# Performance work log

Measured on AMD Instinct MI355X. Metric: run time of the kernel, lower is better.

The kernel has to match this reference:

```python
import jax, jax.numpy as jnp
import numpy as np

K = 4
REG_MAX = 32


def setup_inputs() -> dict:
    key = jax.random.key(0)
    ks = jax.random.split(key, 6)
    B, L, C = 8, 100000, 80
    scores = jax.random.normal(ks[0], (B, L, C), dtype=jnp.float32)
    pred_corners = jax.random.normal(ks[1], (B, L, 4 * (REG_MAX + 1)), dtype=jnp.float32)
    in_dim = 4 * (K + 1)  # 20
    hidden = 64
    w1 = jax.random.normal(ks[2], (in_dim, hidden), dtype=jnp.float32) * (1.0 / np.sqrt(in_dim))
    b1 = jax.random.normal(ks[3], (hidden,), dtype=jnp.float32) * 0.01
    w2 = jax.random.normal(ks[4], (hidden, 1), dtype=jnp.float32) * (1.0 / np.sqrt(hidden))
    b2 = jax.random.normal(ks[5], (1,), dtype=jnp.float32) * 0.01
    return {"scores": scores, "pred_corners": pred_corners,
            "w1": w1, "b1": b1, "w2": w2, "b2": b2}


def reference(scores, pred_corners, w1, b1, w2, b2):
    B, L, _ = pred_corners.shape
    # [B, L, 4, reg_max+1]
    prob = jax.nn.softmax(pred_corners.reshape(B, L, 4, REG_MAX + 1), axis=-1)
    topk, _ = jax.lax.top_k(prob, K)                       # [B, L, 4, k]
    stat = jnp.concatenate([topk, topk.mean(-1, keepdims=True)], axis=-1)  # [B, L, 4, k+1]
    stat = stat.reshape(B, L, 4 * (K + 1))                 # [B, L, 20]
    h = jax.nn.silu(stat @ w1 + b1)                        # [B, L, 64]
    quality = h @ w2 + b2                                  # [B, L, 1]
    return scores + quality
```

## Files before the change

### kernel.cpp

```cpp
#include <hip/hip_runtime.h>

#define LOG2E 1.4426950408889634f

typedef __attribute__((address_space(3))) unsigned int lds_u32_t;
typedef const __attribute__((address_space(1))) unsigned int glb_u32_t;

__global__ __launch_bounds__(256, 4) void lqe_fused2(
    const float* __restrict__ scores,
    const float* __restrict__ pred,
    const float* __restrict__ w1,
    const float* __restrict__ b1,
    const float* __restrict__ w2,
    const float* __restrict__ b2,
    float* __restrict__ out)
{
    __shared__ float predS[64 * 132];
    __shared__ float wS[1412];
    __shared__ float qS[64];

    const int t   = threadIdx.x;
    const int bid = blockIdx.x;

    const size_t f4base = (size_t)bid * 1280;
    const float4* sv4 = reinterpret_cast<const float4*>(scores) + f4base;
    float4 sv[5];
#pragma unroll
    for (int k = 0; k < 5; ++k) sv[k] = sv4[t + 256 * k];

    {
        const float* gp  = pred + (size_t)bid * 8448;
        const int wbase  = t & ~63;
        const int lane   = t & 63;
#pragma unroll
        for (int k = 0; k < 8; ++k) {
            const int f4 = 256 * k + wbase;
            __builtin_amdgcn_global_load_lds(
                (glb_u32_t*)(gp + 4 * (f4 + lane)),
                (lds_u32_t*)(predS + 4 * f4),
                16, 0, 0);
        }
        if (t < 64) {
            __builtin_amdgcn_global_load_lds(
                (glb_u32_t*)(gp + 4 * (2048 + lane)),
                (lds_u32_t*)(predS + 4 * 2048),
                16, 0, 0);
        }
    }

#pragma unroll
    for (int k = 0; k < 5; ++k) wS[t + 256 * k] = w1[t + 256 * k];
    if (t < 64)  { wS[1280 + t] = b1[t]; wS[1344 + t] = w2[t]; }
    if (t == 0)  { wS[1408] = b2[0]; }

    __syncthreads();

    const int r = t >> 2;
    const int c = t & 3;
    const float* xp = predS + r * 132 + c * 33;
    float xs[33];
#pragma unroll
    for (int j = 0; j < 33; ++j) xs[j] = xp[j];

    float t0 = -1e30f, t1 = -1e30f, t2 = -1e30f, t3 = -1e30f;
#pragma unroll
    for (int j = 0; j < 33; ++j) {
        float v  = xs[j];
        float r0 = fminf(t0, v);  t0 = fmaxf(t0, v);
        float r1 = fminf(t1, r0); t1 = fmaxf(t1, r0);
        float r2 = fminf(t2, r1); t2 = fmaxf(t2, r1);
        t3 = fmaxf(t3, r2);
    }

    float denom = 0.f;
#pragma unroll
    for (int j = 0; j < 33; ++j)
        denom += __builtin_amdgcn_exp2f((xs[j] - t0) * LOG2E);
    float rd = __builtin_amdgcn_rcpf(denom);

    float s5[5];
    s5[0] = rd;
    s5[1] = __builtin_amdgcn_exp2f((t1 - t0) * LOG2E) * rd;
    s5[2] = __builtin_amdgcn_exp2f((t2 - t0) * LOG2E) * rd;
    s5[3] = __builtin_amdgcn_exp2f((t3 - t0) * LOG2E) * rd;
    s5[4] = (s5[0] + s5[1] + s5[2] + s5[3]) * 0.25f;

    const int qbase = (t & 63) & ~3;
    float stat[20];
#pragma unroll
    for (int i = 0; i < 20; ++i)
        stat[i] = __shfl(s5[i % 5], qbase + i / 5, 64);

    float hacc[16];
    {
        const float4* b1v = reinterpret_cast<const float4*>(wS + 1280 + 16 * c);
#pragma unroll
        for (int k = 0; k < 4; ++k) {
            float4 b = b1v[k];
            hacc[4*k+0] = b.x; hacc[4*k+1] = b.y; hacc[4*k+2] = b.z; hacc[4*k+3] = b.w;
        }
    }
#pragma unroll
    for (int i = 0; i < 20; ++i) {
        const float si = stat[i];
        const float4* wv = reinterpret_cast<const float4*>(wS + i * 64 + 16 * c);
#pragma unroll
        for (int k = 0; k < 4; ++k) {
            float4 w = wv[k];
            hacc[4*k+0] = fmaf(si, w.x, hacc[4*k+0]);
            hacc[4*k+1] = fmaf(si, w.y, hacc[4*k+1]);
            hacc[4*k+2] = fmaf(si, w.z, hacc[4*k+2]);
            hacc[4*k+3] = fmaf(si, w.w, hacc[4*k+3]);
        }
    }

    float q = 0.f;
    {
        const float4* w2v = reinterpret_cast<const float4*>(wS + 1344 + 16 * c);
#pragma unroll
        for (int k = 0; k < 4; ++k) {
            float4 w = w2v[k];
#pragma unroll
            for (int e = 0; e < 4; ++e) {
                float v  = hacc[4*k+e];
                float sg = __builtin_amdgcn_rcpf(1.f + __builtin_amdgcn_exp2f(-v * LOG2E));
                float we = (e == 0) ? w.x : (e == 1) ? w.y : (e == 2) ? w.z : w.w;
                q = fmaf(v * sg, we, q);
            }
        }
    }
    q += __shfl_xor(q, 1, 64);
    q += __shfl_xor(q, 2, 64);
    q += wS[1408];
    if (c == 0) qS[r] = q;
    __syncthreads();

    float4* ov4 = reinterpret_cast<float4*>(out) + f4base;
#pragma unroll
    for (int k = 0; k < 5; ++k) {
        const int idx = t + 256 * k;
        const float qq = qS[idx / 20];
        float4 s = sv[k];
        s.x += qq; s.y += qq; s.z += qq; s.w += qq;
        ov4[idx] = s;
    }
}

extern "C" void kernel_launch(void* const* d_in, const int* in_sizes, int n_in,
                              void* d_out, int out_size, void* d_ws, size_t ws_size,
                              hipStream_t stream) {
    const float* scores = (const float*)d_in[0];
    const float* pred   = (const float*)d_in[1];
    const float* w1     = (const float*)d_in[2];
    const float* b1     = (const float*)d_in[3];
    const float* w2     = (const float*)d_in[4];
    const float* b2     = (const float*)d_in[5];
    float* out = (float*)d_out;

    const int nrows = in_sizes[1] / 132;
    const int grid  = nrows / 64;

    hipLaunchKernelGGL(lqe_fused2, dim3(grid), dim3(256), 0, stream,
                       scores, pred, w1, b1, w2, b2, out);
}
```

Baseline: 176.0 us.

## Convert to persistent grid with double-buffered LDS prefetch of pred tiles

Replaces the one-tile-per-block launch with a persistent grid of 1024 blocks of 128 threads that each loop over 32-row tiles. The next tile's pred data is staged into a second LDS buffer with global_load_lds while the current tile is computed, and manual vmcnt/lgkmcnt waits plus barriers coordinate the buffers. The goal is to overlap memory fetch with the softmax/top-k/MLP work on this bandwidth-bound kernel. The manual waitcnt counting is fragile, and the last tile issues a redundant reload.

New measurement: 202.7 us. +15.2%, slower.

```diff
diff --git a/kernel.cpp b/kernel.cpp
--- a/kernel.cpp
+++ b/kernel.cpp
@@ -1,147 +1,156 @@
 #include <hip/hip_runtime.h>
 
 #define LOG2E 1.4426950408889634f
+#define ROWS  32
+#define BLK   128
+#define PREDF (ROWS * 132)
+#define SCOR4 (ROWS * 20)
 
 typedef __attribute__((address_space(3))) unsigned int lds_u32_t;
 typedef const __attribute__((address_space(1))) unsigned int glb_u32_t;
 
-__global__ __launch_bounds__(256, 4) void lqe_fused2(
+__device__ __forceinline__ void stage_pred(const float* gp, float* buf, int wv, int lane) {
+#pragma unroll
+    for (int k = 0; k < 8; ++k) {
+        const int f4 = wv * 528 + 64 * k;
+        __builtin_amdgcn_global_load_lds((glb_u32_t*)(gp + 4 * f4 + 4 * lane),
+                                         (lds_u32_t*)(buf + 4 * f4), 16, 0, 0);
+    }
+    const int fb = (wv * 528 + 512) * 4;
+    __builtin_amdgcn_global_load_lds((glb_u32_t*)(gp + fb + lane),
+                                     (lds_u32_t*)(buf + fb), 4, 0, 0);
+}
+
+__global__ __launch_bounds__(BLK, 2) void lqe_pipe(
     const float* __restrict__ scores,
     const float* __restrict__ pred,
     const float* __restrict__ w1,
     const float* __restrict__ b1,
     const float* __restrict__ w2,
     const float* __restrict__ b2,
-    float* __restrict__ out)
+    float* __restrict__ out,
+    int ntiles)
 {
-    __shared__ float predS[64 * 132];
+    __shared__ float predS[2][PREDF];
     __shared__ float wS[1412];
-    __shared__ float qS[64];
+    __shared__ float qS[2][ROWS];
 
-    const int t   = threadIdx.x;
-    const int bid = blockIdx.x;
+    const int t    = threadIdx.x;
+    const int lane = t & 63;
+    const int wv   = t >> 6;
 
-    const size_t f4base = (size_t)bid * 1280;
-    const float4* sv4 = reinterpret_cast<const float4*>(scores) + f4base;
-    float4 sv[5];
-#pragma unroll
-    for (int k = 0; k < 5; ++k) sv[k] = sv4[t + 256 * k];
-
-    {
-        const float* gp  = pred + (size_t)bid * 8448;
-        const int wbase  = t & ~63;
-        const int lane   = t & 63;
-#pragma unroll
-        for (int k = 0; k < 8; ++k) {
-            const int f4 = 256 * k + wbase;
-            __builtin_amdgcn_global_load_lds(
-                (glb_u32_t*)(gp + 4 * (f4 + lane)),
-                (lds_u32_t*)(predS + 4 * f4),
-                16, 0, 0);
-        }
-        if (t < 64) {
-            __builtin_amdgcn_global_load_lds(
-                (glb_u32_t*)(gp + 4 * (2048 + lane)),
-                (lds_u32_t*)(predS + 4 * 2048),
-                16, 0, 0);
-        }
-    }
-
-#pragma unroll
-    for (int k = 0; k < 5; ++k) wS[t + 256 * k] = w1[t + 256 * k];
-    if (t < 64)  { wS[1280 + t] = b1[t]; wS[1344 + t] = w2[t]; }
-    if (t == 0)  { wS[1408] = b2[0]; }
-
+    for (int k = t; k < 1280; k += BLK) wS[k] = w1[k];
+    if (t < 64) { wS[1280 + t] = b1[t]; wS[1344 + t] = w2[t]; }
+    if (t == 0) wS[1408] = b2[0];
     __syncthreads();
 
-    const int r = t >> 2;
-    const int c = t & 3;
-    const float* xp = predS + r * 132 + c * 33;
-    float xs[33];
+    const int stride = gridDim.x;
+    int cur = 0;
+
+    stage_pred(pred + (size_t)blockIdx.x * PREDF, &predS[0][0], wv, lane);
+
+    for (int tile = blockIdx.x; tile < ntiles; tile += stride) {
+        const int nt = (tile + stride < ntiles) ? (tile + stride) : tile;
+
+        const float4* sp = reinterpret_cast<const float4*>(scores) + (size_t)tile * SCOR4;
+        float4 sv0 = sp[t +   0], sv1 = sp[t + 128], sv2 = sp[t + 256],
+               sv3 = sp[t + 384], sv4 = sp[t + 512];
+        stage_pred(pred + (size_t)nt * PREDF, &predS[cur ^ 1][0], wv, lane);
+
+        asm volatile("s_waitcnt vmcnt(14)" ::: "memory");
+        __builtin_amdgcn_sched_barrier(0);
+        __builtin_amdgcn_s_barrier();
+
+        const int r = t >> 2, c = t & 3;
+        const float* xp = &predS[cur][0] + r * 132 + c * 33;
+        float xs[33];
 #pragma unroll
-    for (int j = 0; j < 33; ++j) xs[j] = xp[j];
+        for (int j = 0; j < 33; ++j) xs[j] = xp[j];
 
-    float t0 = -1e30f, t1 = -1e30f, t2 = -1e30f, t3 = -1e30f;
+        float t0 = -1e30f, t1 = -1e30f, t2 = -1e30f, t3 = -1e30f;
 #pragma unroll
-    for (int j = 0; j < 33; ++j) {
-        float v  = xs[j];
-        float r0 = fminf(t0, v);  t0 = fmaxf(t0, v);
-        float r1 = fminf(t1, r0); t1 = fmaxf(t1, r0);
-        float r2 = fminf(t2, r1); t2 = fmaxf(t2, r1);
-        t3 = fmaxf(t3, r2);
-    }
+        for (int j = 0; j < 33; ++j) {
+            float v  = xs[j];
+            float r0 = fminf(t0, v);  t0 = fmaxf(t0, v);
+            float r1 = fminf(t1, r0); t1 = fmaxf(t1, r0);
+            float r2 = fminf(t2, r1); t2 = fmaxf(t2, r1);
+            t3 = fmaxf(t3, r2);
+        }
+        float denom = 0.f;
+#pragma unroll
+        for (int j = 0; j < 33; ++j)
+            denom += __builtin_amdgcn_exp2f((xs[j] - t0) * LOG2E);
+        float rd = __builtin_amdgcn_rcpf(denom);
 
-    float denom = 0.f;
+        float s5[5];
+        s5[0] = rd;
+        s5[1] = __builtin_amdgcn_exp2f((t1 - t0) * LOG2E) * rd;
+        s5[2] = __builtin_amdgcn_exp2f((t2 - t0) * LOG2E) * rd;
+        s5[3] = __builtin_amdgcn_exp2f((t3 - t0) * LOG2E) * rd;
+        s5[4] = (s5[0] + s5[1] + s5[2] + s5[3]) * 0.25f;
+
+        const int qbase = lane & ~3;
+        float stat[20];
 #pragma unroll
-    for (int j = 0; j < 33; ++j)
-        denom += __builtin_amdgcn_exp2f((xs[j] - t0) * LOG2E);
-    float rd = __builtin_amdgcn_rcpf(denom);
+        for (int i = 0; i < 20; ++i)
+            stat[i] = __shfl(s5[i % 5], qbase + i / 5, 64);
 
-    float s5[5];
-    s5[0] = rd;
-    s5[1] = __builtin_amdgcn_exp2f((t1 - t0) * LOG2E) * rd;
-    s5[2] = __builtin_amdgcn_exp2f((t2 - t0) * LOG2E) * rd;
-    s5[3] = __builtin_amdgcn_exp2f((t3 - t0) * LOG2E) * rd;
-    s5[4] = (s5[0] + s5[1] + s5[2] + s5[3]) * 0.25f;
-
-    const int qbase = (t & 63) & ~3;
-    float stat[20];
+        float hacc[16];
+        {
+            const float4* b1v = reinterpret_cast<const float4*>(wS + 1280 + 16 * c);
 #pragma unroll
-    for (int i = 0; i < 20; ++i)
-        stat[i] = __shfl(s5[i % 5], qbase + i / 5, 64);
-
-    float hacc[16];
-    {
-        const float4* b1v = reinterpret_cast<const float4*>(wS + 1280 + 16 * c);
-#pragma unroll
-        for (int k = 0; k < 4; ++k) {
-            float4 b = b1v[k];
-            hacc[4*k+0] = b.x; hacc[4*k+1] = b.y; hacc[4*k+2] = b.z; hacc[4*k+3] = b.w;
-        }
-    }
-#pragma unroll
-    for (int i = 0; i < 20; ++i) {
-        const float si = stat[i];
-        const float4* wv = reinterpret_cast<const float4*>(wS + i * 64 + 16 * c);
-#pragma unroll
-        for (int k = 0; k < 4; ++k) {
-            float4 w = wv[k];
-            hacc[4*k+0] = fmaf(si, w.x, hacc[4*k+0]);
-            hacc[4*k+1] = fmaf(si, w.y, hacc[4*k+1]);
-            hacc[4*k+2] = fmaf(si, w.z, hacc[4*k+2]);
-            hacc[4*k+3] = fmaf(si, w.w, hacc[4*k+3]);
-        }
-    }
-
-    float q = 0.f;
-    {
-        const float4* w2v = reinterpret_cast<const float4*>(wS + 1344 + 16 * c);
-#pragma unroll
-        for (int k = 0; k < 4; ++k) {
-            float4 w = w2v[k];
-#pragma unroll
-            for (int e = 0; e < 4; ++e) {
-                float v  = hacc[4*k+e];
-                float sg = __builtin_amdgcn_rcpf(1.f + __builtin_amdgcn_exp2f(-v * LOG2E));
-                float we = (e == 0) ? w.x : (e == 1) ? w.y : (e == 2) ? w.z : w.w;
-                q = fmaf(v * sg, we, q);
+            for (int k = 0; k < 4; ++k) {
+                float4 b = b1v[k];
+                hacc[4*k+0]=b.x; hacc[4*k+1]=b.y; hacc[4*k+2]=b.z; hacc[4*k+3]=b.w;
             }
         }
-    }
-    q += __shfl_xor(q, 1, 64);
-    q += __shfl_xor(q, 2, 64);
-    q += wS[1408];
-    if (c == 0) qS[r] = q;
-    __syncthreads();
+#pragma unroll
+        for (int i = 0; i < 20; ++i) {
+            const float si = stat[i];
+            const float4* wv4 = reinterpret_cast<const float4*>(wS + i * 64 + 16 * c);
+#pragma unroll
+            for (int k = 0; k < 4; ++k) {
+                float4 w = wv4[k];
+                hacc[4*k+0] = fmaf(si, w.x, hacc[4*k+0]);
+                hacc[4*k+1] = fmaf(si, w.y, hacc[4*k+1]);
+                hacc[4*k+2] = fmaf(si, w.z, hacc[4*k+2]);
+                hacc[4*k+3] = fmaf(si, w.w, hacc[4*k+3]);
+            }
+        }
+        float q = 0.f;
+        {
+            const float4* w2v = reinterpret_cast<const float4*>(wS + 1344 + 16 * c);
+#pragma unroll
+            for (int k = 0; k < 4; ++k) {
+                float4 w = w2v[k];
+#pragma unroll
+                for (int e = 0; e < 4; ++e) {
+                    float v  = hacc[4*k+e];
+                    float sg = __builtin_amdgcn_rcpf(1.f + __builtin_amdgcn_exp2f(-v * LOG2E));
+                    float we = (e == 0) ? w.x : (e == 1) ? w.y : (e == 2) ? w.z : w.w;
+                    q = fmaf(v * sg, we, q);
+                }
+            }
+        }
+        q += __shfl_xor(q, 1, 64);
+        q += __shfl_xor(q, 2, 64);
+        q += wS[1408];
+        if (c == 0) qS[cur][r] = q;
 
-    float4* ov4 = reinterpret_cast<float4*>(out) + f4base;
-#pragma unroll
-    for (int k = 0; k < 5; ++k) {
-        const int idx = t + 256 * k;
-        const float qq = qS[idx / 20];
-        float4 s = sv[k];
-        s.x += qq; s.y += qq; s.z += qq; s.w += qq;
-        ov4[idx] = s;
+        asm volatile("s_waitcnt lgkmcnt(0)" ::: "memory");
+        __builtin_amdgcn_sched_barrier(0);
+        __builtin_amdgcn_s_barrier();
+
+        float4* op = reinterpret_cast<float4*>(out) + (size_t)tile * SCOR4;
+        {
+            float qq;
+            qq = qS[cur][(t +   0) / 20]; sv0.x+=qq; sv0.y+=qq; sv0.z+=qq; sv0.w+=qq; op[t +   0] = sv0;
+            qq = qS[cur][(t + 128) / 20]; sv1.x+=qq; sv1.y+=qq; sv1.z+=qq; sv1.w+=qq; op[t + 128] = sv1;
+            qq = qS[cur][(t + 256) / 20]; sv2.x+=qq; sv2.y+=qq; sv2.z+=qq; sv2.w+=qq; op[t + 256] = sv2;
+            qq = qS[cur][(t + 384) / 20]; sv3.x+=qq; sv3.y+=qq; sv3.z+=qq; sv3.w+=qq; op[t + 384] = sv3;
+            qq = qS[cur][(t + 512) / 20]; sv4.x+=qq; sv4.y+=qq; sv4.z+=qq; sv4.w+=qq; op[t + 512] = sv4;
+        }
+        cur ^= 1;
     }
 }
 
@@ -156,9 +165,10 @@
     const float* b2     = (const float*)d_in[5];
     float* out = (float*)d_out;
 
-    const int nrows = in_sizes[1] / 132;
-    const int grid  = nrows / 64;
+    const int nrows  = in_sizes[1] / 132;
+    const int ntiles = nrows / ROWS;
+    const int grid   = 1024;
 
-    hipLaunchKernelGGL(lqe_fused2, dim3(grid), dim3(256), 0, stream,
-                       scores, pred, w1, b1, w2, b2, out);
+    hipLaunchKernelGGL(lqe_pipe, dim3(grid), dim3(BLK), 0, stream,
+                       scores, pred, w1, b1, w2, b2, out, ntiles);
 }
```

## Make each wave own its 16 rows and drop the block barrier

Applied to the files above, without the earlier changes.

Each wavefront now loads its own 16-row slice of pred into a private LDS region, waits on vmcnt only for its own loads, and writes its output using in-wave shuffles instead of a shared qS array. This removes the second __syncthreads so waves proceed independently after the weight load. Scores are now loaded after the pred wait instead of being issued up front, which may lose some overlap. The occupancy hint in launch_bounds is also removed.

After: 172.5 us. 1.02x faster.

```diff
diff --git a/kernel.cpp b/kernel.cpp
--- a/kernel.cpp
+++ b/kernel.cpp
@@ -5,7 +5,7 @@
 typedef __attribute__((address_space(3))) unsigned int lds_u32_t;
 typedef const __attribute__((address_space(1))) unsigned int glb_u32_t;
 
-__global__ __launch_bounds__(256, 4) void lqe_fused2(
+__global__ __launch_bounds__(256) void lqe_wave(
     const float* __restrict__ scores,
     const float* __restrict__ pred,
     const float* __restrict__ w1,
@@ -14,49 +14,43 @@
     const float* __restrict__ b2,
     float* __restrict__ out)
 {
-    __shared__ float predS[64 * 132];
-    __shared__ float wS[1412];
-    __shared__ float qS[64];
+    __shared__ __align__(16) float predS[4 * 2112];
+    __shared__ __align__(16) float wS[1412];
 
-    const int t   = threadIdx.x;
-    const int bid = blockIdx.x;
-
-    const size_t f4base = (size_t)bid * 1280;
-    const float4* sv4 = reinterpret_cast<const float4*>(scores) + f4base;
-    float4 sv[5];
-#pragma unroll
-    for (int k = 0; k < 5; ++k) sv[k] = sv4[t + 256 * k];
-
-    {
-        const float* gp  = pred + (size_t)bid * 8448;
-        const int wbase  = t & ~63;
-        const int lane   = t & 63;
-#pragma unroll
-        for (int k = 0; k < 8; ++k) {
-            const int f4 = 256 * k + wbase;
-            __builtin_amdgcn_global_load_lds(
-                (glb_u32_t*)(gp + 4 * (f4 + lane)),
-                (lds_u32_t*)(predS + 4 * f4),
-                16, 0, 0);
-        }
-        if (t < 64) {
-            __builtin_amdgcn_global_load_lds(
-                (glb_u32_t*)(gp + 4 * (2048 + lane)),
-                (lds_u32_t*)(predS + 4 * 2048),
-                16, 0, 0);
-        }
-    }
+    const int t    = threadIdx.x;
+    const int lane = t & 63;
+    const int wv   = t >> 6;
+    const int tile = blockIdx.x;
 
 #pragma unroll
     for (int k = 0; k < 5; ++k) wS[t + 256 * k] = w1[t + 256 * k];
-    if (t < 64)  { wS[1280 + t] = b1[t]; wS[1344 + t] = w2[t]; }
-    if (t == 0)  { wS[1408] = b2[0]; }
-
+    if (t < 64) { wS[1280 + t] = b1[t]; wS[1344 + t] = w2[t]; }
+    if (t == 0) wS[1408] = b2[0];
     __syncthreads();
 
-    const int r = t >> 2;
-    const int c = t & 3;
-    const float* xp = predS + r * 132 + c * 33;
+    const float* gp  = pred + (size_t)tile * 8448 + wv * 2112;
+    float*       buf = predS + wv * 2112;
+#pragma unroll
+    for (int k = 0; k < 8; ++k) {
+        __builtin_amdgcn_global_load_lds((glb_u32_t*)(gp + 256 * k + 4 * lane),
+                                         (lds_u32_t*)(buf + 256 * k), 16, 0, 0);
+    }
+    __builtin_amdgcn_global_load_lds((glb_u32_t*)(gp + 2048 + lane),
+                                     (lds_u32_t*)(buf + 2048), 4, 0, 0);
+
+    asm volatile("s_waitcnt vmcnt(0)" ::: "memory");
+    __builtin_amdgcn_sched_barrier(0);
+
+    const size_t s4 = (size_t)tile * 1280 + wv * 320;
+    const float4* sp = reinterpret_cast<const float4*>(scores) + s4;
+    float4 sv0 = sp[lane +   0];
+    float4 sv1 = sp[lane +  64];
+    float4 sv2 = sp[lane + 128];
+    float4 sv3 = sp[lane + 192];
+    float4 sv4 = sp[lane + 256];
+
+    const int r = lane >> 2, c = lane & 3;
+    const float* xp = buf + r * 132 + c * 33;
     float xs[33];
 #pragma unroll
     for (int j = 0; j < 33; ++j) xs[j] = xp[j];
@@ -70,7 +64,6 @@
         float r2 = fminf(t2, r1); t2 = fmaxf(t2, r1);
         t3 = fmaxf(t3, r2);
     }
-
     float denom = 0.f;
 #pragma unroll
     for (int j = 0; j < 33; ++j)
@@ -84,11 +77,10 @@
     s5[3] = __builtin_amdgcn_exp2f((t3 - t0) * LOG2E) * rd;
     s5[4] = (s5[0] + s5[1] + s5[2] + s5[3]) * 0.25f;
 
-    const int qbase = (t & 63) & ~3;
     float stat[20];
 #pragma unroll
     for (int i = 0; i < 20; ++i)
-        stat[i] = __shfl(s5[i % 5], qbase + i / 5, 64);
+        stat[i] = __shfl(s5[i % 5], i / 5, 4);
 
     float hacc[16];
     {
@@ -96,23 +88,22 @@
 #pragma unroll
         for (int k = 0; k < 4; ++k) {
             float4 b = b1v[k];
-            hacc[4*k+0] = b.x; hacc[4*k+1] = b.y; hacc[4*k+2] = b.z; hacc[4*k+3] = b.w;
+            hacc[4*k+0]=b.x; hacc[4*k+1]=b.y; hacc[4*k+2]=b.z; hacc[4*k+3]=b.w;
         }
     }
 #pragma unroll
     for (int i = 0; i < 20; ++i) {
         const float si = stat[i];
-        const float4* wv = reinterpret_cast<const float4*>(wS + i * 64 + 16 * c);
+        const float4* wv4 = reinterpret_cast<const float4*>(wS + i * 64 + 16 * c);
 #pragma unroll
         for (int k = 0; k < 4; ++k) {
-            float4 w = wv[k];
+            float4 w = wv4[k];
             hacc[4*k+0] = fmaf(si, w.x, hacc[4*k+0]);
             hacc[4*k+1] = fmaf(si, w.y, hacc[4*k+1]);
             hacc[4*k+2] = fmaf(si, w.z, hacc[4*k+2]);
             hacc[4*k+3] = fmaf(si, w.w, hacc[4*k+3]);
         }
     }
-
     float q = 0.f;
     {
         const float4* w2v = reinterpret_cast<const float4*>(wS + 1344 + 16 * c);
@@ -128,20 +119,23 @@
             }
         }
     }
-    q += __shfl_xor(q, 1, 64);
-    q += __shfl_xor(q, 2, 64);
+    q += __shfl_xor(q, 1, 4);
+    q += __shfl_xor(q, 2, 4);
     q += wS[1408];
-    if (c == 0) qS[r] = q;
-    __syncthreads();
 
-    float4* ov4 = reinterpret_cast<float4*>(out) + f4base;
-#pragma unroll
-    for (int k = 0; k < 5; ++k) {
-        const int idx = t + 256 * k;
-        const float qq = qS[idx / 20];
-        float4 s = sv[k];
-        s.x += qq; s.y += qq; s.z += qq; s.w += qq;
-        ov4[idx] = s;
+    float4* op = reinterpret_cast<float4*>(out) + s4;
+    {
+        float qq; int idx, rl;
+        idx = lane +   0; rl = idx / 20; qq = __shfl(q, rl * 4, 64);
+        sv0.x+=qq; sv0.y+=qq; sv0.z+=qq; sv0.w+=qq; op[idx] = sv0;
+        idx = lane +  64; rl = idx / 20; qq = __shfl(q, rl * 4, 64);
+        sv1.x+=qq; sv1.y+=qq; sv1.z+=qq; sv1.w+=qq; op[idx] = sv1;
+        idx = lane + 128; rl = idx / 20; qq = __shfl(q, rl * 4, 64);
+        sv2.x+=qq; sv2.y+=qq; sv2.z+=qq; sv2.w+=qq; op[idx] = sv2;
+        idx = lane + 192; rl = idx / 20; qq = __shfl(q, rl * 4, 64);
+        sv3.x+=qq; sv3.y+=qq; sv3.z+=qq; sv3.w+=qq; op[idx] = sv3;
+        idx = lane + 256; rl = idx / 20; qq = __shfl(q, rl * 4, 64);
+        sv4.x+=qq; sv4.y+=qq; sv4.z+=qq; sv4.w+=qq; op[idx] = sv4;
     }
 }
 
@@ -159,6 +153,6 @@
     const int nrows = in_sizes[1] / 132;
     const int grid  = nrows / 64;
 
-    hipLaunchKernelGGL(lqe_fused2, dim3(grid), dim3(256), 0, stream,
+    hipLaunchKernelGGL(lqe_wave, dim3(grid), dim3(256), 0, stream,
                        scores, pred, w1, b1, w2, b2, out);
 }
```
